# Optimization experiments

Hardware: AMD Instinct MI355X
Metric: run time of the kernel (lower is better)

## Reference

```python
import jax, jax.numpy as jnp
import numpy as np

N, T, E = 20000, 4, 320000
IN_F, H_F, OUT_F, HEADS = 32, 16, 16, 8
NEG_SLOPE = 0.2


def gat_layer(x, W, al, ar, b, src, dst, n_nodes, heads, f_out):
    # x: [N, T, Fin], W: [Fin, heads*f_out], al/ar: [heads, f_out], b: [heads*f_out]
    feat = (x @ W).reshape(x.shape[0], x.shape[1], heads, f_out)      # [N,T,H,F]
    el = (feat * al).sum(-1)                                          # [N,T,H]
    er = (feat * ar).sum(-1)                                          # [N,T,H]
    e = jax.nn.leaky_relu(el[src] + er[dst], NEG_SLOPE)               # [E,T,H]
    # segment softmax over incoming edges of each destination node
    m = jax.lax.stop_gradient(jax.ops.segment_max(e, dst, num_segments=n_nodes))
    ex = jnp.exp(e - m[dst])
    s = jax.ops.segment_sum(ex, dst, num_segments=n_nodes)
    alpha = ex / s[dst]                                               # [E,T,H]
    msg = feat[src] * alpha[..., None]                                # [E,T,H,F]
    out = jax.ops.segment_sum(msg, dst, num_segments=n_nodes)
    return out + b.reshape(1, 1, heads, f_out)


def setup_inputs() -> dict:
    key = jax.random.key(0)
    ks = jax.random.split(key, 12)
    x = jax.random.normal(ks[0], (N, T, IN_F), dtype=jnp.float32)
    src = jax.random.randint(ks[1], (E,), 0, N)
    dst = jax.random.randint(ks[2], (E,), 0, N)
    s = 0.1
    W1 = jax.random.normal(ks[3], (IN_F, HEADS * H_F), dtype=jnp.float32) * s
    al1 = jax.random.normal(ks[4], (HEADS, H_F), dtype=jnp.float32) * s
    ar1 = jax.random.normal(ks[5], (HEADS, H_F), dtype=jnp.float32) * s
    b1 = jnp.zeros((HEADS * H_F,), dtype=jnp.float32)
    W2 = jax.random.normal(ks[6], (HEADS * H_F, OUT_F), dtype=jnp.float32) * s
    al2 = jax.random.normal(ks[7], (1, OUT_F), dtype=jnp.float32) * s
    ar2 = jax.random.normal(ks[8], (1, OUT_F), dtype=jnp.float32) * s
    b2 = jnp.zeros((OUT_F,), dtype=jnp.float32)
    return {"x": x, "src": src, "dst": dst, "W1": W1, "al1": al1, "ar1": ar1,
            "b1": b1, "W2": W2, "al2": al2, "ar2": ar2, "b2": b2}


def reference(x, src, dst, W1, al1, ar1, b1, W2, al2, ar2, b2):
    n = x.shape[0]
    h = gat_layer(x, W1, al1, ar1, b1, src, dst, n, HEADS, H_F)   # [N,T,H,F]
    h = h.reshape(n, h.shape[1], -1)                              # [N,T,H*F]
    h = gat_layer(h, W2, al2, ar2, b2, src, dst, n, 1, OUT_F)     # [N,T,1,OUT]
    return h.squeeze(2)                                           # [N,T,OUT]
```

## Files before the change

kernel.cpp:

```cpp
#include <hip/hip_runtime.h>
#include <hip/hip_fp16.h>
#include <math.h>

#define NN 20000
#define TT 4
#define EE 320000
#define NT (NN*TT)
#define H1 8
#define C1 128
#define IN_F 32
#define OUT_F 16
#define CAP 96
#define SCAT_BLOCKS 313
#define XCAST_BLOCKS 1250

typedef _Float16 h8 __attribute__((ext_vector_type(8)));
typedef float f32x4 __attribute__((ext_vector_type(4)));

__device__ __forceinline__ float lrelu_exp(float e) {
  e = (e >= 0.f) ? e : 0.2f * e;
  return __expf(e);
}

__global__ __launch_bounds__(256) void k_front(
    const float* __restrict__ x, const float* __restrict__ W1,
    const float* __restrict__ al1, const float* __restrict__ ar1,
    const float* __restrict__ W2, const float* __restrict__ al2,
    const float* __restrict__ ar2,
    const int4* __restrict__ src4, const int4* __restrict__ dst4,
    int* __restrict__ cnt, int* __restrict__ csr96,
    __half* __restrict__ xh, float* __restrict__ el1, float* __restrict__ er1,
    __half* __restrict__ W1hp, __half* __restrict__ W2pp) {
  __shared__ h8 ELERs[64];
  int b = blockIdx.x;
  int tid = threadIdx.x;
  if (b < SCAT_BLOCKS) {
    int e4 = b * 256 + tid;
    if (e4 < EE / 4) {
      int4 s = src4[e4];
      int4 d = dst4[e4];
      int p0 = atomicAdd(&cnt[d.x], 1); csr96[d.x * CAP + p0] = s.x;
      int p1 = atomicAdd(&cnt[d.y], 1); csr96[d.y * CAP + p1] = s.y;
      int p2 = atomicAdd(&cnt[d.z], 1); csr96[d.z * CAP + p2] = s.z;
      int p3 = atomicAdd(&cnt[d.w], 1); csr96[d.w * CAP + p3] = s.w;
    }
    return;
  }
  if (b == SCAT_BLOCKS) {
    for (int idx = tid; idx < 8 * 512; idx += 256) {
      int tile = idx >> 9;
      int rem = idx & 511;
      int lane = rem >> 3, j = rem & 7;
      int k = (lane >> 4) * 8 + j;
      int n = lane & 15;
      W1hp[idx] = __float2half(W1[k * C1 + tile * 16 + n]);
    }
    for (int idx = tid; idx < 8 * 512; idx += 256) {
      int tile = idx >> 9;
      int rem = idx & 511;
      int lane = rem >> 3, j = rem & 7;
      int ks = tile & 3;
      int k = ks * 32 + (lane >> 4) * 8 + j;
      int n = lane & 15;
      float v = 0.f;
      if (tile < 4) {
        v = W2[k * OUT_F + n];
      } else if (n == 0) {
        float s = 0.f;
        for (int f = 0; f < 16; ++f) s += W2[k * OUT_F + f] * al2[f];
        v = s;
      } else if (n == 1) {
        float s = 0.f;
        for (int f = 0; f < 16; ++f) s += W2[k * OUT_F + f] * ar2[f];
        v = s;
      }
      W2pp[idx] = __float2half(v);
    }
    return;
  }
  {
    __half* E = (__half*)ELERs;
    for (int idx = tid; idx < 512; idx += 256) {
      int lane = idx >> 3, j = idx & 7;
      int k = (lane >> 4) * 8 + j;
      int n = lane & 15;
      int hh_ = n & 7;
      const float* a = (n < 8) ? al1 : ar1;
      float s = 0.f;
      for (int f = 0; f < 16; ++f) s += W1[k * C1 + hh_ * 16 + f] * a[hh_ * 16 + f];
      E[idx] = __float2half(s);
    }
  }
  __syncthreads();
  int wave = tid >> 6, lane = tid & 63;
  int m = lane & 15, quad = lane >> 4;
  int rowbase = (b - SCAT_BLOCKS - 1) * 64 + wave * 16;
  int row = rowbase + m;
  const float4* xp = (const float4*)(x + row * IN_F + quad * 8);
  float4 a0 = xp[0], a1 = xp[1];
  h8 af;
  af[0] = (_Float16)a0.x; af[1] = (_Float16)a0.y;
  af[2] = (_Float16)a0.z; af[3] = (_Float16)a0.w;
  af[4] = (_Float16)a1.x; af[5] = (_Float16)a1.y;
  af[6] = (_Float16)a1.z; af[7] = (_Float16)a1.w;
  *(h8*)(xh + (size_t)row * IN_F + quad * 8) = af;
  {
    h8 bf = ELERs[lane];
    f32x4 c = {0.f, 0.f, 0.f, 0.f};
    c = __builtin_amdgcn_mfma_f32_16x16x32_f16(af, bf, c, 0, 0, 0);
#pragma unroll
    for (int r = 0; r < 4; ++r) {
      int orow = rowbase + quad * 4 + r;
      if (m < 8) el1[orow * H1 + m] = c[r];
      else       er1[orow * H1 + (m - 8)] = c[r];
    }
  }
}

__global__ __launch_bounds__(256, 4) void k_agg1m(
    const __half* __restrict__ xh,
    const float* __restrict__ el1,
    const float* __restrict__ er1,
    const int* __restrict__ cnt, const int* __restrict__ csr96,
    const __half* __restrict__ W1hp, const float* __restrict__ b1,
    const __half* __restrict__ W2pp,
    __half* __restrict__ feat2h, float* __restrict__ el2,
    float* __restrict__ er2) {
  __shared__ int4 stg4[4][384];
  __shared__ __half axs[16][264];
  __shared__ __half hs[16][136];
  int tid = threadIdx.x;
  int wv = tid >> 6, lane = tid & 63;
  int n = blockIdx.x * 4 + wv;
  int slot = lane >> 1;
  int t = lane >> 4;
  int hf = lane & 1;
  float er_i = er1[(size_t)n * 32 + slot];
  int deg = cnt[n];
  const int* eb = csr96 + (size_t)n * CAP;
  const char* el1b = (const char*)el1;
  const char* xhb  = (const char*)xh;
  char* myst = (char*)stg4[wv];
  h8 accA = {0, 0, 0, 0, 0, 0, 0, 0};
  h8 accB = {0, 0, 0, 0, 0, 0, 0, 0};
  float l = 0.f;
  for (int chunk = 0; chunk < deg; chunk += 64) {
    int m64 = min(64, deg - chunk);
    int sv = (lane < m64) ? eb[chunk + lane] : 0;
    int nq = (m64 + 15) >> 4;
    for (int q = 0; q < nq; ++q) {
      int mc = min(16, m64 - q * 16);
      int4 st[6];
#pragma unroll
      for (int i = 0; i < 6; ++i) {
        int g = i * 64 + lane;
        int e = g / 24;
        int seg = g - e * 24;
        int ec = (e < mc) ? e : (mc - 1);
        int s = __builtin_amdgcn_ds_bpermute(((q << 4) + ec) << 2, sv);
        const char* p = (seg < 8)
            ? (el1b + (size_t)s * 128 + seg * 16)
            : (xhb  + (size_t)s * 256 + (seg - 8) * 16);
        st[i] = *(const int4*)p;
      }
#pragma unroll
      for (int i = 0; i < 6; ++i)
        *(int4*)(myst + i * 1024 + lane * 16) = st[i];
#pragma unroll
      for (int e = 0; e < 16; ++e) {
        float ew = *(const float*)(myst + e * 384 + slot * 4);
        h8 xa = *(const h8*)(myst + e * 384 + 128 + t * 64 + hf * 32);
        h8 xb = *(const h8*)(myst + e * 384 + 128 + t * 64 + hf * 32 + 16);
        float w_ = lrelu_exp(ew + er_i);
        w_ = (e < mc) ? w_ : 0.f;
        l += w_;
        _Float16 wh_ = (_Float16)w_;
        h8 w8_ = {wh_, wh_, wh_, wh_, wh_, wh_, wh_, wh_};
        accA += w8_ * xa;
        accB += w8_ * xb;
      }
    }
  }
  float inv = (l > 0.f) ? (1.f / l) : 0.f;
  {
    h8 r0, r1;
#pragma unroll
    for (int q = 0; q < 8; ++q) {
      r0[q] = (_Float16)((float)accA[q] * inv);
      r1[q] = (_Float16)((float)accB[q] * inv);
    }
    int hh_ = slot & 7;
    __half* op = &axs[wv * 4 + t][hh_ * 32 + hf * 16];
    *(h8*)op = r0;
    *(h8*)(op + 8) = r1;
  }
  __syncthreads();

  int m = lane & 15, quad = lane >> 4;
  const h8* bp1 = (const h8*)W1hp;
#pragma unroll
  for (int hi = 0; hi < 2; ++hi) {
    int head = wv * 2 + hi;
    h8 af = *(const h8*)&axs[m][head * 32 + quad * 8];
    f32x4 c = {0.f, 0.f, 0.f, 0.f};
    c = __builtin_amdgcn_mfma_f32_16x16x32_f16(af, bp1[head * 64 + lane], c, 0, 0, 0);
    float bv = b1[head * 16 + m];
#pragma unroll
    for (int r = 0; r < 4; ++r)
      hs[quad * 4 + r][head * 16 + m] = __float2half(c[r] + bv);
  }
  __syncthreads();
  if (wv != 0) return;
  const h8* bp2 = (const h8*)W2pp;
  f32x4 cF = {0.f, 0.f, 0.f, 0.f};
  f32x4 cE = {0.f, 0.f, 0.f, 0.f};
#pragma unroll
  for (int ks = 0; ks < 4; ++ks) {
    h8 af = *(const h8*)&hs[m][ks * 32 + quad * 8];
    cF = __builtin_amdgcn_mfma_f32_16x16x32_f16(af, bp2[ks * 64 + lane], cF, 0, 0, 0);
    cE = __builtin_amdgcn_mfma_f32_16x16x32_f16(af, bp2[(4 + ks) * 64 + lane], cE, 0, 0, 0);
  }
#pragma unroll
  for (int r = 0; r < 4; ++r) {
    int orow = blockIdx.x * 16 + quad * 4 + r;
    feat2h[(size_t)orow * OUT_F + m] = __float2half(cF[r]);
    if (m == 0) el2[orow] = cE[r];
    if (m == 1) er2[orow] = cE[r];
  }
}

__global__ __launch_bounds__(256, 4) void k_agg2x(
    const __half* __restrict__ feat2h,
    const float* __restrict__ el2, const float* __restrict__ er2,
    const int* __restrict__ cnt, const int* __restrict__ csr96,
    const float* __restrict__ b2, float* __restrict__ out) {
  __shared__ int4 stg4[4][192];
  int tid = threadIdx.x;
  int wv = tid >> 6, lane = tid & 63;
  int n = blockIdx.x * 4 + wv;
  int t = lane >> 4, f = lane & 15;
  float ern = er2[n * 4 + t];
  int deg = cnt[n];
  const int* eb = csr96 + (size_t)n * CAP;
  const char* f2b = (const char*)feat2h;
  const char* e2b = (const char*)el2;
  char* myst = (char*)stg4[wv];
  float acc = 0.f, l = 0.f;
  for (int chunk = 0; chunk < deg; chunk += 64) {
    int m64 = min(64, deg - chunk);
    int sv = (lane < m64) ? eb[chunk + lane] : 0;
    int nq = (m64 + 15) >> 4;
    for (int q = 0; q < nq; ++q) {
      int mc = min(16, m64 - q * 16);
      int4 st[3];
#pragma unroll
      for (int i = 0; i < 3; ++i) {
        int g = i * 64 + lane;
        int e = g / 9;
        int seg = g - e * 9;
        if (e > 15) { e = 15; seg = 8; }
        int ec = (e < mc) ? e : (mc - 1);
        int s = __builtin_amdgcn_ds_bpermute(((q << 4) + ec) << 2, sv);
        const char* p = (seg < 8)
            ? (f2b + (size_t)s * 128 + seg * 16)
            : (e2b + (size_t)s * 16);
        st[i] = *(const int4*)p;
      }
#pragma unroll
      for (int i = 0; i < 3; ++i)
        *(int4*)(myst + i * 1024 + lane * 16) = st[i];
#pragma unroll
      for (int e = 0; e < 16; ++e) {
        float ew = *(const float*)(myst + e * 144 + 128 + t * 4);
        __half fv = *(const __half*)(myst + e * 144 + t * 32 + f * 2);
        float w_ = lrelu_exp(ew + ern);
        w_ = (e < mc) ? w_ : 0.f;
        l += w_;
        acc = fmaf(w_, __half2float(fv), acc);
      }
    }
  }
  float inv = (l > 0.f) ? (1.f / l) : 0.f;
  out[(size_t)(n * 4 + t) * OUT_F + f] = acc * inv + b2[f];
}

extern "C" void kernel_launch(void* const* d_in, const int* in_sizes, int n_in,
                              void* d_out, int out_size, void* d_ws, size_t ws_size,
                              hipStream_t stream) {
  const float* x   = (const float*)d_in[0];
  const int*   src = (const int*)d_in[1];
  const int*   dst = (const int*)d_in[2];
  const float* W1  = (const float*)d_in[3];
  const float* al1 = (const float*)d_in[4];
  const float* ar1 = (const float*)d_in[5];
  const float* b1  = (const float*)d_in[6];
  const float* W2  = (const float*)d_in[7];
  const float* al2 = (const float*)d_in[8];
  const float* ar2 = (const float*)d_in[9];
  const float* b2  = (const float*)d_in[10];
  float* out = (float*)d_out;

  char* w = (char*)d_ws;
  __half* xh     = (__half*)w; w += (size_t)NT * IN_F * 2;
  __half* feat2h = (__half*)w; w += (size_t)NT * OUT_F * 2;
  float*  el1    = (float*)w;  w += (size_t)NT * H1 * 4;
  float*  er1    = (float*)w;  w += (size_t)NT * H1 * 4;
  float*  el2    = (float*)w;  w += (size_t)NT * 4;
  float*  er2    = (float*)w;  w += (size_t)NT * 4;
  __half* W1hp   = (__half*)w; w += (size_t)8 * 512 * 2;
  __half* W2pp   = (__half*)w; w += (size_t)8 * 512 * 2;
  int* cnt     = (int*)w;      w += (size_t)NN * 4;
  int* csr96   = (int*)w;      w += (size_t)NN * CAP * 4;

  hipMemsetAsync(cnt, 0, NN * sizeof(int), stream);

  k_front<<<SCAT_BLOCKS + 1 + XCAST_BLOCKS, 256, 0, stream>>>(
      x, W1, al1, ar1, W2, al2, ar2, (const int4*)src, (const int4*)dst,
      cnt, csr96, xh, el1, er1, W1hp, W2pp);
  k_agg1m<<<NN / 4, 256, 0, stream>>>(xh, el1, er1, cnt, csr96,
                                      W1hp, b1, W2pp, feat2h, el2, er2);
  k_agg2x<<<NN / 4, 256, 0, stream>>>(feat2h, el2, er2, cnt, csr96, b2, out);
}
```

Baseline: 168.9 us.

## Gather neighbor features directly from global memory instead of LDS staging

The layer-1 aggregation kernel no longer stages 16 edges' el1/xh rows cooperatively into shared memory before consuming them. Each lane now reads four neighbor indices with readlane and loads its own el1 scalar and two h8 feature vectors straight from global memory, processing four edges per iteration. This removes LDS round-trips, the bpermute shuffles and the shared staging buffer, and the occupancy hint is dropped from launch bounds. In exchange, global loads become narrower and more scattered, and there is less memory-level parallelism per iteration.

```diff
diff --git a/kernel.cpp b/kernel.cpp
--- a/kernel.cpp
+++ b/kernel.cpp
@@ -117,7 +117,7 @@
   }
 }
 
-__global__ __launch_bounds__(256, 4) void k_agg1m(
+__global__ __launch_bounds__(256) void k_agg1m(
     const __half* __restrict__ xh,
     const float* __restrict__ el1,
     const float* __restrict__ er1,
@@ -126,7 +126,6 @@
     const __half* __restrict__ W2pp,
     __half* __restrict__ feat2h, float* __restrict__ el2,
     float* __restrict__ er2) {
-  __shared__ int4 stg4[4][384];
   __shared__ __half axs[16][264];
   __shared__ __half hs[16][136];
   int tid = threadIdx.x;
@@ -138,47 +137,44 @@
   float er_i = er1[(size_t)n * 32 + slot];
   int deg = cnt[n];
   const int* eb = csr96 + (size_t)n * CAP;
-  const char* el1b = (const char*)el1;
-  const char* xhb  = (const char*)xh;
-  char* myst = (char*)stg4[wv];
   h8 accA = {0, 0, 0, 0, 0, 0, 0, 0};
   h8 accB = {0, 0, 0, 0, 0, 0, 0, 0};
   float l = 0.f;
   for (int chunk = 0; chunk < deg; chunk += 64) {
-    int m64 = min(64, deg - chunk);
-    int sv = (lane < m64) ? eb[chunk + lane] : 0;
-    int nq = (m64 + 15) >> 4;
-    for (int q = 0; q < nq; ++q) {
-      int mc = min(16, m64 - q * 16);
-      int4 st[6];
-#pragma unroll
-      for (int i = 0; i < 6; ++i) {
-        int g = i * 64 + lane;
-        int e = g / 24;
-        int seg = g - e * 24;
-        int ec = (e < mc) ? e : (mc - 1);
-        int s = __builtin_amdgcn_ds_bpermute(((q << 4) + ec) << 2, sv);
-        const char* p = (seg < 8)
-            ? (el1b + (size_t)s * 128 + seg * 16)
-            : (xhb  + (size_t)s * 256 + (seg - 8) * 16);
-        st[i] = *(const int4*)p;
+    int m = min(64, deg - chunk);
+    int sv = (lane < m) ? eb[chunk + lane] : 0;
+    int iters = (m + 3) >> 2;
+    for (int g = 0; g < iters; ++g) {
+      int j = g * 4;
+      int s0 = __builtin_amdgcn_readlane(sv, j + 0);
+      int s1 = __builtin_amdgcn_readlane(sv, j + 1);
+      int s2 = __builtin_amdgcn_readlane(sv, j + 2);
+      int s3 = __builtin_amdgcn_readlane(sv, j + 3);
+      float ew0 = el1[(size_t)s0 * 32 + slot];
+      float ew1 = el1[(size_t)s1 * 32 + slot];
+      float ew2 = el1[(size_t)s2 * 32 + slot];
+      float ew3 = el1[(size_t)s3 * 32 + slot];
+      const __half* x0 = xh + (size_t)(s0 * 4 + t) * 32 + hf * 16;
+      const __half* x1 = xh + (size_t)(s1 * 4 + t) * 32 + hf * 16;
+      const __half* x2 = xh + (size_t)(s2 * 4 + t) * 32 + hf * 16;
+      const __half* x3 = xh + (size_t)(s3 * 4 + t) * 32 + hf * 16;
+      h8 a0 = *(const h8*)x0, b0 = *(const h8*)(x0 + 8);
+      h8 a1 = *(const h8*)x1, b1_ = *(const h8*)(x1 + 8);
+      h8 a2 = *(const h8*)x2, b2_ = *(const h8*)(x2 + 8);
+      h8 a3 = *(const h8*)x3, b3_ = *(const h8*)(x3 + 8);
+#define CONSUME(K, EW, XA, XB)                                    \
+      {                                                           \
+        float w_ = lrelu_exp(EW + er_i);                          \
+        w_ = (j + K < m) ? w_ : 0.f;                              \
+        l += w_;                                                  \
+        _Float16 wh_ = (_Float16)w_;                              \
+        h8 w8_ = {wh_, wh_, wh_, wh_, wh_, wh_, wh_, wh_};        \
+        accA += w8_ * XA;                                         \
+        accB += w8_ * XB;                                         \
       }
-#pragma unroll
-      for (int i = 0; i < 6; ++i)
-        *(int4*)(myst + i * 1024 + lane * 16) = st[i];
-#pragma unroll
-      for (int e = 0; e < 16; ++e) {
-        float ew = *(const float*)(myst + e * 384 + slot * 4);
-        h8 xa = *(const h8*)(myst + e * 384 + 128 + t * 64 + hf * 32);
-        h8 xb = *(const h8*)(myst + e * 384 + 128 + t * 64 + hf * 32 + 16);
-        float w_ = lrelu_exp(ew + er_i);
-        w_ = (e < mc) ? w_ : 0.f;
-        l += w_;
-        _Float16 wh_ = (_Float16)w_;
-        h8 w8_ = {wh_, wh_, wh_, wh_, wh_, wh_, wh_, wh_};
-        accA += w8_ * xa;
-        accB += w8_ * xb;
-      }
+      CONSUME(0, ew0, a0, b0) CONSUME(1, ew1, a1, b1_)
+      CONSUME(2, ew2, a2, b2_) CONSUME(3, ew3, a3, b3_)
+#undef CONSUME
     }
   }
   float inv = (l > 0.f) ? (1.f / l) : 0.f;
```

New measurement: 150.6 us. 10.8% less time.
